# Optimization experiments

Hardware: AMD Instinct MI355X
Metric: run time of the kernel (lower is better)

The kernel has to match this reference:

```python
import jax, jax.numpy as jnp
import numpy as np

B, T, D, H, L, V = 2, 1024, 1024, 16, 6, 32000
HD = D // H  # head_size = n_emb // n_heads
EPS = 1e-5   # torch LayerNorm default


def setup_inputs() -> dict:
    key = jax.random.key(0)
    ks = jax.random.split(key, 19)
    s = 0.02
    n = lambda k, shape: jax.random.normal(k, shape, dtype=jnp.float32) * s
    return {
        "idx": jax.random.randint(ks[0], (B, T), 0, V),
        "targets": jax.random.randint(ks[1], (B, T), 0, V),
        "tok_emb": n(ks[2], (V, D)),
        "pos_emb": n(ks[3], (V, D)),  # only first T rows used, as in the source
        "Wq": n(ks[4], (L, H, D, HD)),
        "Wk": n(ks[5], (L, H, D, HD)),
        "Wv": n(ks[6], (L, H, D, HD)),
        "Wo": n(ks[7], (L, D, D)),
        "bo": n(ks[8], (L, D)),
        "W1": n(ks[9], (L, D, 4 * D)),
        "b1": n(ks[10], (L, 4 * D)),
        "W2": n(ks[11], (L, 4 * D, D)),
        "b2": n(ks[12], (L, D)),
        "ln_g": jnp.ones((D,), jnp.float32),
        "ln_b": jnp.zeros((D,), jnp.float32),
        "Wf": n(ks[13], (D, V)),
        "bf": n(ks[14], (V,)),
    }


def _layer_norm(x, g, b):
    mu = jnp.mean(x, axis=-1, keepdims=True)
    var = jnp.mean(jnp.square(x - mu), axis=-1, keepdims=True)
    return (x - mu) * jax.lax.rsqrt(var + EPS) * g + b


def _forward(idx, targets, tok_emb, pos_emb, Wq, Wk, Wv, Wo, bo,
             W1, b1, W2, b2, ln_g, ln_b, Wf, bf):
    x = tok_emb[idx] + pos_emb[:T]  # [B,T,D]
    tril = jnp.tril(jnp.ones((T, T), dtype=bool))
    scale = jnp.asarray(D, x.dtype) ** -0.5  # NOTE: source scales by C=N_EMBED, not head_size

    def block(x, p):
        wq, wk, wv, wo, bo_, w1, b1_, w2, b2_ = p
        q = jnp.einsum('btd,hde->bhte', x, wq)
        k = jnp.einsum('btd,hde->bhte', x, wk)
        v = jnp.einsum('btd,hde->bhte', x, wv)
        scores = jnp.einsum('bhte,bhse->bhts', q, k) * scale
        scores = jnp.where(tril, scores, -jnp.inf)
        att = jax.nn.softmax(scores, axis=-1)
        o = jnp.einsum('bhts,bhse->bhte', att, v)
        o = o.transpose(0, 2, 1, 3).reshape(B, T, D)  # concat heads
        x = x + o @ wo + bo_                           # attn residual (no LN in source)
        h = jax.nn.relu(x @ w1 + b1_)
        x = x + h @ w2 + b2_                           # ffn residual
        return x, None

    x, _ = jax.lax.scan(block, x, (Wq, Wk, Wv, Wo, bo, W1, b1, W2, b2))
    x = _layer_norm(x, ln_g, ln_b)
    logits = x @ Wf + bf  # [B,T,V]
    logp = jax.nn.log_softmax(logits, axis=-1)
    nll = -jnp.take_along_axis(logp, targets[..., None], axis=-1)
    loss = jnp.mean(nll)
    return logits, loss


def reference(idx, targets, tok_emb, pos_emb, Wq, Wk, Wv, Wo, bo,
              W1, b1, W2, b2, ln_g, ln_b, Wf, bf):
    return _forward(idx, targets, tok_emb, pos_emb, Wq, Wk, Wv, Wo, bo,
                    W1, b1, W2, b2, ln_g, ln_b, Wf, bf)
```

## Files before the change

kernel.cpp:

```cpp
#include <hip/hip_runtime.h>
#include <hip/hip_bf16.h>

typedef unsigned short u16;
typedef unsigned int u32;
typedef float f32x4 __attribute__((ext_vector_type(4)));
typedef __bf16 bf16x8 __attribute__((ext_vector_type(8)));

#define NB 2
#define NT 1024
#define ND 1024
#define NH 16
#define HDIM 64
#define NL 6
#define NV 32000
#define ND4 4096
#define BT (NB * NT)
#define L2E 1.44269504f
#define NSLOT 500

__device__ __forceinline__ u16 f2b(float f) {
  u32 u = __builtin_bit_cast(u32, f);
  u32 r = (u + 0x7FFFu + ((u >> 16) & 1u)) >> 16;
  return (u16)r;
}

__device__ __forceinline__ void gl_lds16(const void* g, void* lds) {
  __builtin_amdgcn_global_load_lds((const __attribute__((address_space(1))) u32*)g,
                                   (__attribute__((address_space(3))) u32*)lds, 16, 0, 0);
}

__device__ __forceinline__ float rmax16(float v) {
  v = fmaxf(v, __shfl_xor(v, 1, 64));
  v = fmaxf(v, __shfl_xor(v, 2, 64));
  v = fmaxf(v, __shfl_xor(v, 4, 64));
  v = fmaxf(v, __shfl_xor(v, 8, 64));
  return v;
}
__device__ __forceinline__ float rsum16(float v) {
  v += __shfl_xor(v, 1, 64);
  v += __shfl_xor(v, 2, 64);
  v += __shfl_xor(v, 4, 64);
  v += __shfl_xor(v, 8, 64);
  return v;
}

__global__ void k_embed(const int* __restrict__ idx, const float* __restrict__ tok,
                        const float* __restrict__ pos, float* __restrict__ xf,
                        u16* __restrict__ xb) {
  int row = blockIdx.x;
  int t = row & (NT - 1);
  int tk = idx[row];
  int c = threadIdx.x * 4;
  float4 a = *(const float4*)(tok + (size_t)tk * ND + c);
  float4 p = *(const float4*)(pos + (size_t)t * ND + c);
  float4 s = make_float4(a.x + p.x, a.y + p.y, a.z + p.z, a.w + p.w);
  *(float4*)(xf + (size_t)row * ND + c) = s;
  u16* o = xb + (size_t)row * ND + c;
  *(u32*)(o + 0) = (u32)f2b(s.x) | ((u32)f2b(s.y) << 16);
  *(u32*)(o + 2) = (u32)f2b(s.z) | ((u32)f2b(s.w) << 16);
}

__device__ __forceinline__ void tr_tile(const float* in, int in_rs, u16* out, int out_rs,
                                        int k0, int n0, float (*t)[65]) {
  int tid = threadIdx.x;
#pragma unroll
  for (int i = 0; i < 16; ++i) {
    int e = tid + 256 * i;
    int r = e >> 6, c = e & 63;
    t[r][c] = in[(size_t)(k0 + r) * in_rs + n0 + c];
  }
  __syncthreads();
#pragma unroll
  for (int i = 0; i < 16; ++i) {
    int e = tid + 256 * i;
    int r = e >> 6, c = e & 63;
    out[(size_t)(n0 + r) * out_rs + k0 + c] = f2b(t[c][r]);
  }
}

__global__ void k_transpose(const float* __restrict__ in, u16* __restrict__ out,
                            int K, int N) {
  __shared__ float t[64][65];
  tr_tile(in, N, out, K, blockIdx.y * 64, blockIdx.x * 64, t);
}

__global__ void k_trans_layer(const float* __restrict__ Wq, const float* __restrict__ Wk,
                              const float* __restrict__ Wv, const float* __restrict__ Wo,
                              const float* __restrict__ W1, const float* __restrict__ W2,
                              u16* __restrict__ wqkvT, u16* __restrict__ woT,
                              u16* __restrict__ w1T, u16* __restrict__ w2T, int l) {
  __shared__ float t[64][65];
  int i = blockIdx.x;
  if (i < 768) {
    int x = i & 15, z = i >> 4;
    int s = z >> 4, h = z & 15;
    const float* in = (s == 0 ? Wq : s == 1 ? Wk : Wv) + ((size_t)(l * NH + h)) * ND * HDIM;
    u16* o = wqkvT + ((size_t)(s * ND + h * HDIM)) * ND;
    tr_tile(in, HDIM, o, ND, x * 64, 0, t);
  } else if (i < 1024) {
    int j = i - 768, x = j & 15, y = j >> 4;
    tr_tile(Wo + (size_t)l * ND * ND, ND, woT, ND, y * 64, x * 64, t);
  } else if (i < 2048) {
    int j = i - 1024, x = j & 63, y = j >> 6;
    tr_tile(W1 + (size_t)l * ND * ND4, ND4, w1T, ND, y * 64, x * 64, t);
  } else {
    int j = i - 2048, x = j & 15, y = j >> 4;
    tr_tile(W2 + (size_t)l * ND4 * ND, ND, w2T, ND4, y * 64, x * 64, t);
  }
}

template <int EPI>
__global__ void __launch_bounds__(512, 2)
k_gemm8(const u16* __restrict__ A, const u16* __restrict__ Bt,
        const float* __restrict__ bias, float* __restrict__ outf,
        u16* __restrict__ outb, int K, int N, int nMt, float* __restrict__ pl) {
  __shared__ u16 lds[2][2][2][128 * 64];
  int tid = threadIdx.x;
  int w = tid >> 6, l = tid & 63;
  int l4 = l >> 4, lm = l & 15;
  int wm = w >> 2, wn = w & 3;

  int nwg = gridDim.x, bid = blockIdx.x;
  int q8 = nwg >> 3, r8 = nwg & 7;
  int xcd = bid & 7, loc = bid >> 3;
  int swz = (xcd < r8 ? xcd * (q8 + 1) : r8 * (q8 + 1) + (xcd - r8) * q8) + loc;
  int m0 = (swz % nMt) * 256;
  int n0 = (swz / nMt) * 256;

  f32x4 acc[8][4];
  f32x4 z = {0.f, 0.f, 0.f, 0.f};
#pragma unroll
  for (int m = 0; m < 8; ++m)
#pragma unroll
    for (int n = 0; n < 4; ++n) acc[m][n] = z;

  int srow = (w << 3) + (l >> 3);
  int scol = (((l & 7) ^ ((l >> 3) & 7)) << 3);
  int sdst = w * 512 + l * 8;

  auto stage_half = [&](int b, int mat, int h, int kt) {
    int k0 = kt << 6;
    const u16* base = (mat == 0 ? A + (size_t)(m0 + (h << 7)) * K
                                : Bt + (size_t)(n0 + (h << 7)) * K);
#pragma unroll
    for (int i = 0; i < 2; ++i)
      gl_lds16(base + (size_t)(i * 64 + srow) * K + k0 + scol,
               &lds[b][mat][h][i * 4096 + sdst]);
  };

  int c0 = (l4 ^ (lm & 7)) * 8;
  int c1 = c0 ^ 32;
  int brow0 = (wn & 1) * 64;

  const u16* A0h = &lds[0][0][wm][0];
  const u16* B0h = &lds[0][1][wn >> 1][0];
  const u16* A1h = &lds[1][0][wm][0];
  const u16* B1h = &lds[1][1][wn >> 1][0];

  bf16x8 Ar[4][2], Bx[2][2], By[2][2];

  auto dsA = [&](const u16* Ah, int mf0) {
#pragma unroll
    for (int mf = 0; mf < 4; ++mf) {
      Ar[mf][0] = *(const bf16x8*)&Ah[((mf0 + mf) * 16 + lm) * 64 + c0];
      Ar[mf][1] = *(const bf16x8*)&Ah[((mf0 + mf) * 16 + lm) * 64 + c1];
    }
  };
  auto dsB = [&](const u16* Bh, bf16x8 (&B)[2][2], int nf0) {
#pragma unroll
    for (int nf = 0; nf < 2; ++nf) {
      B[nf][0] = *(const bf16x8*)&Bh[(brow0 + (nf0 + nf) * 16 + lm) * 64 + c0];
      B[nf][1] = *(const bf16x8*)&Bh[(brow0 + (nf0 + nf) * 16 + lm) * 64 + c1];
    }
  };
  auto mm = [&](int am, bf16x8 (&B)[2][2], int an) {
    __builtin_amdgcn_s_setprio(1);
#pragma unroll
    for (int mf = 0; mf < 4; ++mf)
#pragma unroll
      for (int nf = 0; nf < 2; ++nf) {
        acc[am + mf][an + nf] =
            __builtin_amdgcn_mfma_f32_16x16x32_bf16(Ar[mf][0], B[nf][0], acc[am + mf][an + nf], 0, 0, 0);
        acc[am + mf][an + nf] =
            __builtin_amdgcn_mfma_f32_16x16x32_bf16(Ar[mf][1], B[nf][1], acc[am + mf][an + nf], 0, 0, 0);
      }
    __builtin_amdgcn_s_setprio(0);
  };
  auto openbar = [&]() {
    __builtin_amdgcn_sched_barrier(0);
    __builtin_amdgcn_s_barrier();
    __builtin_amdgcn_sched_barrier(0);
  };
  auto midbar = [&]() {
    __builtin_amdgcn_sched_barrier(0);
    __builtin_amdgcn_s_barrier();
    asm volatile("s_waitcnt lgkmcnt(0)" ::: "memory");
    __builtin_amdgcn_sched_barrier(0);
  };

  int nk = K >> 6;
  stage_half(0, 0, 0, 0); stage_half(0, 0, 1, 0);
  stage_half(0, 1, 0, 0); stage_half(0, 1, 1, 0);
  stage_half(1, 0, 0, 1);

  for (int u = 0; u < nk; u += 2) {
    bool s2 = (u + 2 < nk), s3 = (u + 3 < nk);
    asm volatile("s_waitcnt vmcnt(2)" ::: "memory");
    openbar();
    dsA(A0h, 0); dsB(B0h, Bx, 0);
    stage_half(1, 0, 1, u + 1);
    midbar();
    mm(0, Bx, 0);
    openbar();
    dsB(B0h, By, 2);
    stage_half(1, 1, 0, u + 1);
    midbar();
    mm(0, By, 2);
    openbar();
    dsA(A0h, 4);
    stage_half(1, 1, 1, u + 1);
    midbar();
    mm(4, By, 2);
    openbar();
    if (s2) stage_half(0, 0, 0, u + 2);
    midbar();
    mm(4, Bx, 0);
    if (s2) asm volatile("s_waitcnt vmcnt(2)" ::: "memory");
    else    asm volatile("s_waitcnt vmcnt(0)" ::: "memory");
    openbar();
    dsA(A1h, 0); dsB(B1h, Bx, 0);
    if (s2) stage_half(0, 0, 1, u + 2);
    midbar();
    mm(0, Bx, 0);
    openbar();
    dsB(B1h, By, 2);
    if (s2) stage_half(0, 1, 0, u + 2);
    midbar();
    mm(0, By, 2);
    openbar();
    dsA(A1h, 4);
    if (s2) stage_half(0, 1, 1, u + 2);
    midbar();
    mm(4, By, 2);
    openbar();
    if (s3) stage_half(1, 0, 0, u + 3);
    midbar();
    mm(4, Bx, 0);
  }

  if constexpr (EPI == 4) {
    int slot = (n0 >> 6) + wn;
#pragma unroll
    for (int mf = 0; mf < 8; ++mf)
#pragma unroll
      for (int j = 0; j < 4; ++j) {
        int row = m0 + wm * 128 + mf * 16 + l4 * 4 + j;
        float sm = 0.f;
#pragma unroll
        for (int nf = 0; nf < 4; ++nf) {
          int col = n0 + wn * 64 + nf * 16 + lm;
          float v = acc[mf][nf][j] + bias[col];
          outf[(size_t)row * N + col] = v;
          sm += exp2f(v * L2E);
        }
        sm = rsum16(sm);
        if (lm == 0) pl[(size_t)row * NSLOT + slot] = sm;
      }
  } else {
#pragma unroll
    for (int mf = 0; mf < 8; ++mf)
#pragma unroll
      for (int nf = 0; nf < 4; ++nf)
#pragma unroll
        for (int j = 0; j < 4; ++j) {
          int row = m0 + wm * 128 + mf * 16 + l4 * 4 + j;
          int col = n0 + wn * 64 + nf * 16 + lm;
          float v = acc[mf][nf][j];
          if constexpr (EPI == 0) outb[(size_t)row * N + col] = f2b(v);
          else outf[(size_t)row * N + col] = v + bias[col];
        }
  }
}

template <int EPI, int BN>
__global__ void __launch_bounds__(256, BN == 64 ? 3 : 2)
k_gemm4(const u16* __restrict__ A, const u16* __restrict__ Bt,
        const float* __restrict__ bias, float* __restrict__ outf,
        u16* __restrict__ outb, int K, int N, int nMt) {
  constexpr int NFW = BN / 32;
  constexpr int NH2 = NFW / 2;
  __shared__ u16 As[2][128 * 64];
  __shared__ u16 Bs[2][BN * 64];
  int tid = threadIdx.x;
  int w = tid >> 6, l = tid & 63;
  int l4 = l >> 4, lm = l & 15;
  int wr = w >> 1, wc = w & 1;

  int nwg = gridDim.x, bid = blockIdx.x;
  int q8 = nwg >> 3, r8 = nwg & 7;
  int xcd = bid & 7, loc = bid >> 3;
  int swz = (xcd < r8 ? xcd * (q8 + 1) : r8 * (q8 + 1) + (xcd - r8) * q8) + loc;
  int m0 = (swz % nMt) * 128;
  int n0 = (swz / nMt) * BN;

  f32x4 acc[4][NFW];
  f32x4 z = {0.f, 0.f, 0.f, 0.f};
#pragma unroll
  for (int m = 0; m < 4; ++m)
#pragma unroll
    for (int n = 0; n < NFW; ++n) acc[m][n] = z;

  int srow = (w << 3) + (l >> 3);
  int scol = (((l & 7) ^ ((l >> 3) & 7)) << 3);
  int sdst = w * 512 + l * 8;

  const u16* Arow = A + (size_t)m0 * K;
  const u16* Brow = Bt + (size_t)n0 * K;

  auto stage = [&](int b, int kt) {
    int k0 = kt << 6;
#pragma unroll
    for (int i = 0; i < 4; ++i)
      gl_lds16(Arow + (size_t)(i * 32 + srow) * K + k0 + scol, &As[b][i * 2048 + sdst]);
#pragma unroll
    for (int i = 0; i < BN / 32; ++i)
      gl_lds16(Brow + (size_t)(i * 32 + srow) * K + k0 + scol, &Bs[b][i * 2048 + sdst]);
  };

  int c0 = (l4 ^ (lm & 7)) * 8;
  int c1 = c0 ^ 32;

  int nk = K >> 6;
  stage(0, 0);
  for (int t = 0; t < nk; ++t) {
    int b = t & 1;
    asm volatile("s_waitcnt vmcnt(0)" ::: "memory");
    __builtin_amdgcn_sched_barrier(0);
    __builtin_amdgcn_s_barrier();
    __builtin_amdgcn_sched_barrier(0);
    if (t + 1 < nk) stage(b ^ 1, t + 1);
    __builtin_amdgcn_sched_barrier(0);

    bf16x8 af[4][2], bfr[NH2][2];
#pragma unroll
    for (int mf = 0; mf < 4; ++mf) {
      af[mf][0] = *(const bf16x8*)&As[b][(mf * 16 + lm) * 64 + c0 + (wr * 64 * 64)];
      af[mf][1] = *(const bf16x8*)&As[b][(mf * 16 + lm) * 64 + c1 + (wr * 64 * 64)];
    }
#pragma unroll
    for (int nf = 0; nf < NH2; ++nf) {
      int brow = wc * (BN / 2) + nf * 16 + lm;
      bfr[nf][0] = *(const bf16x8*)&Bs[b][brow * 64 + c0];
      bfr[nf][1] = *(const bf16x8*)&Bs[b][brow * 64 + c1];
    }
    __builtin_amdgcn_s_setprio(1);
#pragma unroll
    for (int mf = 0; mf < 4; ++mf)
#pragma unroll
      for (int nf = 0; nf < NH2; ++nf) {
        acc[mf][nf] = __builtin_amdgcn_mfma_f32_16x16x32_bf16(af[mf][0], bfr[nf][0], acc[mf][nf], 0, 0, 0);
        acc[mf][nf] = __builtin_amdgcn_mfma_f32_16x16x32_bf16(af[mf][1], bfr[nf][1], acc[mf][nf], 0, 0, 0);
      }
    __builtin_amdgcn_s_setprio(0);

#pragma unroll
    for (int nf = 0; nf < NH2; ++nf) {
      int brow = wc * (BN / 2) + (nf + NH2) * 16 + lm;
      bfr[nf][0] = *(const bf16x8*)&Bs[b][brow * 64 + c0];
      bfr[nf][1] = *(const bf16x8*)&Bs[b][brow * 64 + c1];
    }
    __builtin_amdgcn_s_setprio(1);
#pragma unroll
    for (int mf = 0; mf < 4; ++mf)
#pragma unroll
      for (int nf = 0; nf < NH2; ++nf) {
        acc[mf][nf + NH2] = __builtin_amdgcn_mfma_f32_16x16x32_bf16(af[mf][0], bfr[nf][0], acc[mf][nf + NH2], 0, 0, 0);
        acc[mf][nf + NH2] = __builtin_amdgcn_mfma_f32_16x16x32_bf16(af[mf][1], bfr[nf][1], acc[mf][nf + NH2], 0, 0, 0);
      }
    __builtin_amdgcn_s_setprio(0);
  }

#pragma unroll
  for (int mf = 0; mf < 4; ++mf)
#pragma unroll
    for (int nf = 0; nf < NFW; ++nf)
#pragma unroll
      for (int j = 0; j < 4; ++j) {
        int row = m0 + wr * 64 + mf * 16 + l4 * 4 + j;
        int col = n0 + wc * (BN / 2) + nf * 16 + lm;
        float v = acc[mf][nf][j];
        if constexpr (EPI == 0) {
          outb[(size_t)row * N + col] = f2b(v);
        } else if constexpr (EPI == 2) {
          v += bias[col];
          outb[(size_t)row * N + col] = f2b(fmaxf(v, 0.f));
        } else {
          v += bias[col];
          size_t o = (size_t)row * N + col;
          float nx = outf[o] + v;
          outf[o] = nx;
          outb[o] = f2b(nx);
        }
      }
}

__global__ void __launch_bounds__(512) k_attn(const u16* __restrict__ qkv,
                                              u16* __restrict__ ob) {
  int bid = blockIdx.x;
  int qb = bid & 7, h = (bid >> 3) & 15, b = bid >> 7;
  int tid = threadIdx.x;
  int w = tid >> 6, l = tid & 63;
  int l4 = l >> 4, lm = l & 15;

  __shared__ u16 Ks[128][72];
  __shared__ u16 Vt[64][136];
  __shared__ u16 Pw[8][16][136];

  const u16* base = qkv + (size_t)b * NT * 3072 + h * HDIM;

  bf16x8 qf[2];
#pragma unroll
  for (int kk = 0; kk < 2; ++kk) {
    int tq = qb * 128 + w * 16 + lm;
    qf[kk] = *(const bf16x8*)(base + (size_t)tq * 3072 + kk * 32 + l4 * 8);
  }

  f32x4 z = {0.f, 0.f, 0.f, 0.f};
  f32x4 oacc[4];
  float mrow[4], lrow[4];
#pragma unroll
  for (int n = 0; n < 4; ++n) oacc[n] = z;
#pragma unroll
  for (int j = 0; j < 4; ++j) { mrow[j] = -1e30f; lrow[j] = 0.f; }

  for (int kb = 0; kb <= qb; ++kb) {
    __syncthreads();
#pragma unroll
    for (int i = 0; i < 2; ++i) {
      int c = tid + 512 * i;
      int r = c >> 3, e0 = (c & 7) << 3;
      const u16* src = base + (size_t)(kb * 128 + r) * 3072;
      *(bf16x8*)&Ks[r][e0] = *(const bf16x8*)(src + 1024 + e0);
      union { bf16x8 v; u16 u[8]; } uu;
      uu.v = *(const bf16x8*)(src + 2048 + e0);
#pragma unroll
      for (int j = 0; j < 8; ++j) Vt[e0 + j][r] = uu.u[j];
    }
    __syncthreads();

    f32x4 s[8];
#pragma unroll
    for (int n = 0; n < 8; ++n) s[n] = z;
#pragma unroll
    for (int kk = 0; kk < 2; ++kk)
#pragma unroll
      for (int n = 0; n < 8; ++n) {
        bf16x8 kf = *(const bf16x8*)&Ks[n * 16 + lm][kk * 32 + l4 * 8];
        s[n] = __builtin_amdgcn_mfma_f32_16x16x32_bf16(qf[kk], kf, s[n], 0, 0, 0);
      }

    bool diag = (kb == qb);
#pragma unroll
    for (int j = 0; j < 4; ++j) {
      int rloc = w * 16 + l4 * 4 + j;
      float pv[8];
      float rm = -1e30f;
#pragma unroll
      for (int n = 0; n < 8; ++n) {
        float vv = s[n][j] * 0.03125f;
        if (diag && (n * 16 + lm > rloc)) vv = -1e30f;
        pv[n] = vv;
        rm = fmaxf(rm, vv);
      }
      rm = rmax16(rm);
      float nm = fmaxf(mrow[j], rm);
      float corr = exp2f((mrow[j] - nm) * L2E);
      mrow[j] = nm;
      float rs = 0.f;
#pragma unroll
      for (int n = 0; n < 8; ++n) {
        float p = exp2f((pv[n] - nm) * L2E);
        pv[n] = p;
        rs += p;
      }
      rs = rsum16(rs);
      lrow[j] = lrow[j] * corr + rs;
#pragma unroll
      for (int n = 0; n < 4; ++n) oacc[n][j] *= corr;
      int prow = l4 * 4 + j;
#pragma unroll
      for (int n = 0; n < 8; ++n) Pw[w][prow][n * 16 + lm] = f2b(pv[n]);
    }
    asm volatile("s_waitcnt lgkmcnt(0)" ::: "memory");
    __builtin_amdgcn_sched_barrier(0);

#pragma unroll
    for (int kk = 0; kk < 4; ++kk) {
      bf16x8 pa = *(const bf16x8*)&Pw[w][lm][kk * 32 + l4 * 8];
#pragma unroll
      for (int n = 0; n < 4; ++n) {
        bf16x8 vf = *(const bf16x8*)&Vt[n * 16 + lm][kk * 32 + l4 * 8];
        oacc[n] = __builtin_amdgcn_mfma_f32_16x16x32_bf16(pa, vf, oacc[n], 0, 0, 0);
      }
    }
  }

#pragma unroll
  for (int n = 0; n < 4; ++n)
#pragma unroll
    for (int j = 0; j < 4; ++j) {
      int tq = qb * 128 + w * 16 + l4 * 4 + j;
      int col = h * HDIM + n * 16 + lm;
      float v = oacc[n][j] / lrow[j];
      ob[(size_t)(b * NT + tq) * ND + col] = f2b(v);
    }
}

__global__ void k_ln(const float* __restrict__ xf, const float* __restrict__ g,
                     const float* __restrict__ bta, u16* __restrict__ xb) {
  __shared__ float red[4];
  int row = blockIdx.x, tid = threadIdx.x;
  int w = tid >> 6;
  int c = tid * 4;
  float4 x = *(const float4*)(xf + (size_t)row * ND + c);
  float s = x.x + x.y + x.z + x.w;
#pragma unroll
  for (int off = 1; off < 64; off <<= 1) s += __shfl_xor(s, off, 64);
  if ((tid & 63) == 0) red[w] = s;
  __syncthreads();
  float mu = (red[0] + red[1] + red[2] + red[3]) * (1.0f / ND);
  float d0 = x.x - mu, d1 = x.y - mu, d2 = x.z - mu, d3 = x.w - mu;
  float v = d0 * d0 + d1 * d1 + d2 * d2 + d3 * d3;
  __syncthreads();
#pragma unroll
  for (int off = 1; off < 64; off <<= 1) v += __shfl_xor(v, off, 64);
  if ((tid & 63) == 0) red[w] = v;
  __syncthreads();
  float var = (red[0] + red[1] + red[2] + red[3]) * (1.0f / ND);
  float rs = rsqrtf(var + 1e-5f);
  float4 gg = *(const float4*)(g + c);
  float4 bb = *(const float4*)(bta + c);
  u16* o = xb + (size_t)row * ND + c;
  o[0] = f2b(d0 * rs * gg.x + bb.x);
  o[1] = f2b(d1 * rs * gg.y + bb.y);
  o[2] = f2b(d2 * rs * gg.z + bb.z);
  o[3] = f2b(d3 * rs * gg.w + bb.w);
}

__global__ void k_loss_row2(const float* __restrict__ pl, const float* __restrict__ logits,
                            const int* __restrict__ tgt, float* __restrict__ lossbuf) {
  int row = blockIdx.x, l = threadIdx.x;
  const float* pr = pl + (size_t)row * NSLOT;
  float s = 0.f;
  for (int i = l; i < NSLOT; i += 64) s += pr[i];
#pragma unroll
  for (int off = 1; off < 64; off <<= 1) s += __shfl_xor(s, off, 64);
  if (l == 0) lossbuf[row] = logf(s) - logits[(size_t)row * NV + tgt[row]];
}

__global__ void k_loss_final(const float* __restrict__ lossbuf, float* __restrict__ out) {
  __shared__ float red[4];
  int tid = threadIdx.x;
  float s = 0.f;
  for (int i = tid; i < BT; i += 256) s += lossbuf[i];
#pragma unroll
  for (int off = 1; off < 64; off <<= 1) s += __shfl_xor(s, off, 64);
  if ((tid & 63) == 0) red[tid >> 6] = s;
  __syncthreads();
  if (tid == 0) out[0] = (red[0] + red[1] + red[2] + red[3]) * (1.0f / BT);
}

extern "C" void kernel_launch(void* const* d_in, const int* in_sizes, int n_in,
                              void* d_out, int out_size, void* d_ws, size_t ws_size,
                              hipStream_t stream) {
  const int* idx = (const int*)d_in[0];
  const int* tgt = (const int*)d_in[1];
  const float* tok = (const float*)d_in[2];
  const float* pos = (const float*)d_in[3];
  const float* Wq = (const float*)d_in[4];
  const float* Wk = (const float*)d_in[5];
  const float* Wv = (const float*)d_in[6];
  const float* Wo = (const float*)d_in[7];
  const float* bo = (const float*)d_in[8];
  const float* W1 = (const float*)d_in[9];
  const float* b1 = (const float*)d_in[10];
  const float* W2 = (const float*)d_in[11];
  const float* b2 = (const float*)d_in[12];
  const float* lng = (const float*)d_in[13];
  const float* lnb = (const float*)d_in[14];
  const float* Wf = (const float*)d_in[15];
  const float* bfp = (const float*)d_in[16];
  float* logits = (float*)d_out;
  float* lossp = logits + (size_t)BT * NV;

  char* ws = (char*)d_ws;
  u16* wT = (u16*)ws;
  size_t off = 65536000;
  float* xf = (float*)(ws + off); off += (size_t)BT * ND * 4;
  u16* xb = (u16*)(ws + off);     off += (size_t)BT * ND * 2;
  u16* qkv = (u16*)(ws + off);    off += (size_t)BT * 3 * ND * 2;
  u16* obuf = (u16*)(ws + off);   off += (size_t)BT * ND * 2;
  u16* hb = (u16*)(ws + off);     off += (size_t)BT * ND4 * 2;
  float* pl = (float*)(ws + off); off += (size_t)BT * NSLOT * 4;
  float* lossbuf = (float*)(ws + off);

  u16* wqkvT = wT;
  u16* woT = wT + (size_t)3 * ND * ND;
  u16* w1T = woT + (size_t)ND * ND;
  u16* w2T = w1T + (size_t)ND4 * ND;

  k_embed<<<BT, 256, 0, stream>>>(idx, tok, pos, xf, xb);
  for (int l = 0; l < NL; ++l) {
    k_trans_layer<<<3072, 256, 0, stream>>>(Wq, Wk, Wv, Wo, W1, W2,
                                            wqkvT, woT, w1T, w2T, l);
    k_gemm4<0, 128><<<384, 256, 0, stream>>>(xb, wqkvT, nullptr, nullptr, qkv, ND, 3 * ND, 16);
    k_attn<<<256, 512, 0, stream>>>(qkv, obuf);
    k_gemm4<3, 64><<<256, 256, 0, stream>>>(obuf, woT, bo + (size_t)l * ND, xf, xb, ND, ND, 16);
    k_gemm4<2, 128><<<512, 256, 0, stream>>>(xb, w1T, b1 + (size_t)l * ND4, nullptr, hb, ND, ND4, 16);
    k_gemm4<3, 64><<<256, 256, 0, stream>>>(hb, w2T, b2 + (size_t)l * ND, xf, xb, ND4, ND, 16);
  }
  k_transpose<<<dim3(500, 16), 256, 0, stream>>>(Wf, wT, ND, NV);
  k_ln<<<BT, 256, 0, stream>>>(xf, lng, lnb, xb);
  k_gemm8<4><<<1000, 512, 0, stream>>>(xb, wT, bfp, logits, nullptr, ND, NV, 8, pl);
  k_loss_row2<<<BT, 64, 0, stream>>>(pl, logits, tgt, lossbuf);
  k_loss_final<<<1, 256, 0, stream>>>(lossbuf, lossp);
}
```

Measured before the change: 1.308 ms.

## Deepen GEMM prefetch pipeline and halve attention query block size

The GEMM kernel now keeps two tiles in flight: a triple buffer for the BN=64 variant, and for BN=128 a double buffer with a second barrier before refilling. Waits use partial vmcnt counts instead of draining all loads, so global-to-LDS loads overlap more with MFMA work. The attention kernel moves to 64-query blocks with 256 threads and 512 workgroups, which gives finer causal load balance and more blocks in flight. In exchange, each K/V tile is loaded by twice as many blocks, and the extra buffers and barriers cost LDS and synchronisation.

```diff
diff --git a/kernel.cpp b/kernel.cpp
--- a/kernel.cpp
+++ b/kernel.cpp
@@ -283,14 +283,15 @@
 }
 
 template <int EPI, int BN>
-__global__ void __launch_bounds__(256, BN == 64 ? 3 : 2)
+__global__ void __launch_bounds__(256, 2)
 k_gemm4(const u16* __restrict__ A, const u16* __restrict__ Bt,
         const float* __restrict__ bias, float* __restrict__ outf,
         u16* __restrict__ outb, int K, int N, int nMt) {
   constexpr int NFW = BN / 32;
   constexpr int NH2 = NFW / 2;
-  __shared__ u16 As[2][128 * 64];
-  __shared__ u16 Bs[2][BN * 64];
+  constexpr int NBUF = (BN == 64) ? 3 : 2;
+  __shared__ u16 As[NBUF][128 * 64];
+  __shared__ u16 Bs[NBUF][BN * 64];
   int tid = threadIdx.x;
   int w = tid >> 6, l = tid & 63;
   int l4 = l >> 4, lm = l & 15;
@@ -330,17 +331,7 @@
   int c0 = (l4 ^ (lm & 7)) * 8;
   int c1 = c0 ^ 32;
 
-  int nk = K >> 6;
-  stage(0, 0);
-  for (int t = 0; t < nk; ++t) {
-    int b = t & 1;
-    asm volatile("s_waitcnt vmcnt(0)" ::: "memory");
-    __builtin_amdgcn_sched_barrier(0);
-    __builtin_amdgcn_s_barrier();
-    __builtin_amdgcn_sched_barrier(0);
-    if (t + 1 < nk) stage(b ^ 1, t + 1);
-    __builtin_amdgcn_sched_barrier(0);
-
+  auto compute = [&](int b) {
     bf16x8 af[4][2], bfr[NH2][2];
 #pragma unroll
     for (int mf = 0; mf < 4; ++mf) {
@@ -362,7 +353,6 @@
         acc[mf][nf] = __builtin_amdgcn_mfma_f32_16x16x32_bf16(af[mf][1], bfr[nf][1], acc[mf][nf], 0, 0, 0);
       }
     __builtin_amdgcn_s_setprio(0);
-
 #pragma unroll
     for (int nf = 0; nf < NH2; ++nf) {
       int brow = wc * (BN / 2) + (nf + NH2) * 16 + lm;
@@ -378,6 +368,33 @@
         acc[mf][nf + NH2] = __builtin_amdgcn_mfma_f32_16x16x32_bf16(af[mf][1], bfr[nf][1], acc[mf][nf + NH2], 0, 0, 0);
       }
     __builtin_amdgcn_s_setprio(0);
+  };
+
+  int nk = K >> 6;
+  stage(0, 0);
+  stage(1, 1);
+  for (int t = 0; t < nk; ++t) {
+    int b = (NBUF == 3) ? (t % 3) : (t & 1);
+    if (t + 1 < nk) {
+      if constexpr (BN == 128) asm volatile("s_waitcnt vmcnt(8)" ::: "memory");
+      else                     asm volatile("s_waitcnt vmcnt(6)" ::: "memory");
+    } else {
+      asm volatile("s_waitcnt vmcnt(0)" ::: "memory");
+    }
+    __builtin_amdgcn_sched_barrier(0);
+    __builtin_amdgcn_s_barrier();
+    __builtin_amdgcn_sched_barrier(0);
+    if constexpr (NBUF == 3) {
+      if (t + 2 < nk) stage((t + 2) % 3, t + 2);
+      __builtin_amdgcn_sched_barrier(0);
+      compute(b);
+    } else {
+      compute(b);
+      __builtin_amdgcn_sched_barrier(0);
+      __builtin_amdgcn_s_barrier();
+      __builtin_amdgcn_sched_barrier(0);
+      if (t + 2 < nk) stage(b, t + 2);
+    }
   }
 
 #pragma unroll
@@ -404,24 +421,24 @@
       }
 }
 
-__global__ void __launch_bounds__(512) k_attn(const u16* __restrict__ qkv,
+__global__ void __launch_bounds__(256) k_attn(const u16* __restrict__ qkv,
                                               u16* __restrict__ ob) {
   int bid = blockIdx.x;
-  int qb = bid & 7, h = (bid >> 3) & 15, b = bid >> 7;
+  int qb = bid & 15, h = (bid >> 4) & 15, b = bid >> 8;
   int tid = threadIdx.x;
   int w = tid >> 6, l = tid & 63;
   int l4 = l >> 4, lm = l & 15;
 
   __shared__ u16 Ks[128][72];
   __shared__ u16 Vt[64][136];
-  __shared__ u16 Pw[8][16][136];
+  __shared__ u16 Pw[4][16][136];
 
   const u16* base = qkv + (size_t)b * NT * 3072 + h * HDIM;
 
   bf16x8 qf[2];
 #pragma unroll
   for (int kk = 0; kk < 2; ++kk) {
-    int tq = qb * 128 + w * 16 + lm;
+    int tq = qb * 64 + w * 16 + lm;
     qf[kk] = *(const bf16x8*)(base + (size_t)tq * 3072 + kk * 32 + l4 * 8);
   }
 
@@ -433,11 +450,12 @@
 #pragma unroll
   for (int j = 0; j < 4; ++j) { mrow[j] = -1e30f; lrow[j] = 0.f; }
 
-  for (int kb = 0; kb <= qb; ++kb) {
+  int nkb = (qb >> 1) + 1;
+  for (int kb = 0; kb < nkb; ++kb) {
     __syncthreads();
 #pragma unroll
-    for (int i = 0; i < 2; ++i) {
-      int c = tid + 512 * i;
+    for (int i = 0; i < 4; ++i) {
+      int c = tid + 256 * i;
       int r = c >> 3, e0 = (c & 7) << 3;
       const u16* src = base + (size_t)(kb * 128 + r) * 3072;
       *(bf16x8*)&Ks[r][e0] = *(const bf16x8*)(src + 1024 + e0);
@@ -459,16 +477,17 @@
         s[n] = __builtin_amdgcn_mfma_f32_16x16x32_bf16(qf[kk], kf, s[n], 0, 0, 0);
       }
 
-    bool diag = (kb == qb);
+    bool diag = (kb == (qb >> 1));
+    int kbase = kb * 128;
 #pragma unroll
     for (int j = 0; j < 4; ++j) {
-      int rloc = w * 16 + l4 * 4 + j;
+      int rglob = qb * 64 + w * 16 + l4 * 4 + j;
       float pv[8];
       float rm = -1e30f;
 #pragma unroll
       for (int n = 0; n < 8; ++n) {
         float vv = s[n][j] * 0.03125f;
-        if (diag && (n * 16 + lm > rloc)) vv = -1e30f;
+        if (diag && (kbase + n * 16 + lm > rglob)) vv = -1e30f;
         pv[n] = vv;
         rm = fmaxf(rm, vv);
       }
@@ -509,7 +528,7 @@
   for (int n = 0; n < 4; ++n)
 #pragma unroll
     for (int j = 0; j < 4; ++j) {
-      int tq = qb * 128 + w * 16 + l4 * 4 + j;
+      int tq = qb * 64 + w * 16 + l4 * 4 + j;
       int col = h * HDIM + n * 16 + lm;
       float v = oacc[n][j] / lrow[j];
       ob[(size_t)(b * NT + tq) * ND + col] = f2b(v);
@@ -614,7 +633,7 @@
     k_trans_layer<<<3072, 256, 0, stream>>>(Wq, Wk, Wv, Wo, W1, W2,
                                             wqkvT, woT, w1T, w2T, l);
     k_gemm4<0, 128><<<384, 256, 0, stream>>>(xb, wqkvT, nullptr, nullptr, qkv, ND, 3 * ND, 16);
-    k_attn<<<256, 512, 0, stream>>>(qkv, obuf);
+    k_attn<<<512, 256, 0, stream>>>(qkv, obuf);
     k_gemm4<3, 64><<<256, 256, 0, stream>>>(obuf, woT, bo + (size_t)l * ND, xf, xb, ND, ND, 16);
     k_gemm4<2, 128><<<512, 256, 0, stream>>>(xb, w1T, b1 + (size_t)l * ND4, nullptr, hb, ND, ND4, 16);
     k_gemm4<3, 64><<<256, 256, 0, stream>>>(hb, w2T, b2 + (size_t)l * ND, xf, xb, ND4, ND, 16);
```

Measured after the change: 1.360 ms. 1.04x slower.
